# Kernel tuning notes

Hardware: AMD Instinct MI355X
Metric: run time of the kernel (lower is better)

The kernel has to match this reference:

```python
import jax, jax.numpy as jnp
import numpy as np

ITERATIONS = 20  # Resonator(iterations=20)
B, F, V, D = 128, 4, 2048, 4096


def _hardsign(x):
    # bipolar normalization used by MAP-VSA multiset(normalize=True); ties -> +1
    return jnp.where(x >= 0, 1.0, -1.0).astype(x.dtype)


def setup_inputs() -> dict:
    key = jax.random.key(0)
    k1, k2 = jax.random.split(key, 2)
    # bipolar codebooks: (F, V, D)
    codebooks = _hardsign(jax.random.normal(k1, (F, V, D), dtype=jnp.float32))
    # a realistic composite input: bind (elementwise product) of one codevector per factor
    idx = jax.random.randint(k2, (B, F), 0, V)                       # (B, F)
    chosen = codebooks[jnp.arange(F)[None, :], idx]                  # (B, F, D)
    inputs = jnp.prod(chosen, axis=1)                                # (B, D)
    # standard resonator init: normalized superposition of each codebook
    init_estimates = jnp.broadcast_to(
        _hardsign(jnp.sum(codebooks, axis=1)), (B, F, D)
    ).astype(jnp.float32)                                            # (B, F, D)
    return {"inputs": inputs, "init_estimates": init_estimates, "codebooks": codebooks}


def _resonator_step(inputs, est, codebooks):
    # est: (B, F, D). rolled stack over k=1..F-1 -> (B, F, F-1, D)
    f = est.shape[-2]
    rolled = jnp.stack([jnp.roll(est, k, axis=-2) for k in range(1, f)], axis=-2)
    inv_others = jnp.prod(rolled, axis=-2)          # multibind over dim -2 -> (B, F, D)
    new_est = inputs[:, None, :] * inv_others       # bind -> (B, F, D)
    sim = jnp.einsum('bfd,fvd->bfv', new_est, codebooks)   # similarity (activation='NONE')
    # multiset(codebooks, sim, normalize=True)
    return _hardsign(jnp.einsum('bfv,fvd->bfd', sim, codebooks))


def reference(inputs, init_estimates, codebooks):
    def body(carry, i):
        est, k, done = carry
        new = _resonator_step(inputs, est, codebooks)
        eq = jnp.all(new == est)          # convergence check (fixed point)
        k = jnp.where(done, k, i)
        return (new, k, done | eq), None

    carry0 = (init_estimates, jnp.int32(0), jnp.bool_(False))
    (est, k, _), _ = jax.lax.scan(body, carry0, jnp.arange(ITERATIONS, dtype=jnp.int32))
    # cleanup: argmax of |similarity| per factor (argmax_abs=True)
    sim = jnp.einsum('bfd,fvd->bfv', est, codebooks)
    outcome = jnp.argmax(jnp.abs(sim), axis=-1)     # (B, F) int indices
    return outcome, k
```

## Files before the change

### kernel.cpp

```cpp
#include <hip/hip_runtime.h>
#include <stdint.h>

#define B_    128
#define F_    4
#define V_    2048
#define D_    4096
#define DW    64
#define VW    32
#define ITERS 20
#define NKT   16
#define NBLK  512
#define ESLOT (B_ * F_ * DW)
#define SSLOT ((size_t)F_ * B_ * V_)

typedef _Float16 half8 __attribute__((ext_vector_type(8)));
typedef float   floatx4 __attribute__((ext_vector_type(4)));

__device__ __forceinline__ void cstore64(uint64_t* p, uint64_t v) {
    __hip_atomic_store(p, v, __ATOMIC_RELAXED, __HIP_MEMORY_SCOPE_AGENT);
}
__device__ __forceinline__ void cstore32(uint32_t* p, uint32_t v) {
    __hip_atomic_store(p, v, __ATOMIC_RELAXED, __HIP_MEMORY_SCOPE_AGENT);
}

__device__ __forceinline__ void xbar(int* bar, int gen) {
    __syncthreads();
    if (threadIdx.x == 0) {
        int s = blockIdx.x & 15;
        int t = __hip_atomic_fetch_add(&bar[s * 16], 1, __ATOMIC_RELAXED,
                                       __HIP_MEMORY_SCOPE_AGENT);
        if (t == gen * (NBLK / 16) - 1)
            __hip_atomic_fetch_add(&bar[256], 1, __ATOMIC_RELAXED,
                                   __HIP_MEMORY_SCOPE_AGENT);
        int spins = 0;
        if (blockIdx.x < 8) {
            while (__hip_atomic_load(&bar[256], __ATOMIC_RELAXED,
                                     __HIP_MEMORY_SCOPE_AGENT) < gen * 16) {
                __builtin_amdgcn_s_sleep(2);
                if (++spins > (1 << 16)) break;
            }
            __hip_atomic_store(&bar[288 + blockIdx.x * 32], gen,
                               __ATOMIC_RELAXED, __HIP_MEMORY_SCOPE_AGENT);
        } else {
            while (__hip_atomic_load(&bar[288 + (blockIdx.x & 7) * 32],
                                     __ATOMIC_RELAXED,
                                     __HIP_MEMORY_SCOPE_AGENT) < gen) {
                __builtin_amdgcn_s_sleep(2);
                if (++spins > (1 << 16)) break;
            }
        }
    }
    __syncthreads();
}

__device__ __forceinline__ void pack32c(const float* __restrict__ x,
                                        uint32_t* __restrict__ bits, int t) {
    const float4* p = (const float4*)x + (size_t)t * 8;
    uint32_t m = 0;
    #pragma unroll
    for (int j = 0; j < 8; ++j) {
        float4 v = p[j];
        m |= (__float_as_uint(v.x) >> 31) << (4 * j + 0);
        m |= (__float_as_uint(v.y) >> 31) << (4 * j + 1);
        m |= (__float_as_uint(v.z) >> 31) << (4 * j + 2);
        m |= (__float_as_uint(v.w) >> 31) << (4 * j + 3);
    }
    cstore32(&bits[t], m);
}

__global__ __launch_bounds__(256, 2) void k_loop(
        const float* __restrict__ cbf, const float* __restrict__ inite,
        const float* __restrict__ inputs,
        uint64_t* __restrict__ cb_bits, uint64_t* __restrict__ cbT,
        uint64_t* __restrict__ est_base, uint64_t* __restrict__ in_bits,
        _Float16* __restrict__ simf_base, int* __restrict__ flags,
        int* __restrict__ keys, int* __restrict__ out, int* bar) {
    const int bid = blockIdx.x;
    const int tid = threadIdx.x;
    const int gtid = bid * 256 + tid;
    int g = 0;

    __shared__ __align__(16) unsigned char LDSU[65536];
    __shared__ uint64_t LUT16[16];
    __shared__ int bd;

    if (tid < 16) {
        uint64_t e = 0;
        #pragma unroll
        for (int j = 0; j < 4; ++j)
            e |= (((tid >> j) & 1) ? 0xBC00ull : 0x3C00ull) << (16 * j);
        LUT16[tid] = e;
    }

    {
        const int ncb = (F_ * V_ * D_) / 32;
        for (int t = gtid; t < ncb; t += NBLK * 256)
            pack32c(cbf, (uint32_t*)cb_bits, t);
        if (gtid < (B_ * F_ * D_) / 32) pack32c(inite, (uint32_t*)est_base, gtid);
        if (gtid < (B_ * D_) / 32)      pack32c(inputs, (uint32_t*)in_bits, gtid);
        if (gtid < 32)      cstore32((uint32_t*)&flags[gtid], 0);
        if (gtid < B_ * F_) cstore32((uint32_t*)&keys[gtid], 0);
    }
    xbar(bar, ++g);

    {
        int wave = tid >> 6, lane = tid & 63;
        #pragma unroll 1
        for (int s = 0; s < 4; ++s) {
            int u = (bid * 4 + wave) + 2048 * s;
            int vw = u & 31, dw = (u >> 5) & 63, f = u >> 11;
            uint64_t w = cb_bits[((size_t)f * V_ + vw * 64 + lane) * DW + dw];
            uint64_t r = 0;
            for (int d2 = 0; d2 < 64; ++d2) {
                uint64_t m = __ballot((unsigned)((w >> d2) & 1));
                if (lane == d2) r = m;
            }
            cstore64(&cbT[((size_t)f * D_ + dw * 64 + lane) * VW + vw], r);
        }
    }
    xbar(bar, ++g);

    const int sgrp = bid & 7;
    const int s_bt = sgrp & 3, s_fhi = sgrp >> 2;
    const int shi  = bid >> 3;
    const int s_vt = shi & 31, s_flo = shi >> 5;
    const int s_f  = s_fhi + 2 * s_flo;
    const int s_v0 = s_vt * 64, s_b0 = s_bt * 32;

    const int ggrp = bid & 7;
    const int g_mt = ggrp & 1, g_f = ggrp >> 1;
    const int g_nt = bid >> 3;
    const int g_m0 = g_mt * 64, g_n0 = g_nt * 64;

    ulonglong2* CB2 = (ulonglong2*)LDSU;
    ulonglong2* NB2 = (ulonglong2*)(LDSU + 32768);
    _Float16*   As  = (_Float16*)(LDSU + 32768);
    uint64_t*   Bb  = (uint64_t*)(LDSU + 49152);

    #pragma unroll
    for (int it = 0; it < 8; ++it) {
        int cq = it * 256 + tid;
        int r = cq >> 5, ch = cq & 31;
        const ulonglong2* src = (const ulonglong2*)(cb_bits + ((size_t)s_f * V_ + s_v0 + r) * DW);
        CB2[r * 32 + (ch ^ (r & 7))] = src[ch];
    }
    {
        const uint64_t* bsrc = cbT + ((size_t)g_f * D_ + g_n0) * VW;
        #pragma unroll
        for (int p = 0; p < 4; ++p) {
            int chunk = p * 256 + tid;
            int dloc = chunk >> 4, cw = chunk & 15;
            ulonglong2 val = *(const ulonglong2*)&bsrc[dloc * VW + cw * 2];
            *(ulonglong2*)&Bb[dloc * VW + ((cw ^ (dloc & 15)) * 2)] = val;
        }
    }

    #pragma unroll 1
    for (int i = 0; i < ITERS; ++i) {
        const uint64_t* esti = est_base + (size_t)i * ESLOT;
        uint64_t*       esto = est_base + (size_t)(i + 1) * ESLOT;
        _Float16*       simf = simf_base + (size_t)i * SSLOT;

        {
            #pragma unroll
            for (int it = 0; it < 4; ++it) {
                int cq = it * 256 + tid;
                int r = cq >> 5, ch = cq & 31;
                int b = s_b0 + r;
                const ulonglong2* iv = (const ulonglong2*)(in_bits + (size_t)b * DW);
                const uint64_t* eb = esti + (size_t)b * F_ * DW;
                ulonglong2 i2 = iv[ch];
                ulonglong2 e0 = ((const ulonglong2*)(eb + 0 * DW))[ch];
                ulonglong2 e1 = ((const ulonglong2*)(eb + 1 * DW))[ch];
                ulonglong2 e2 = ((const ulonglong2*)(eb + 2 * DW))[ch];
                ulonglong2 e3 = ((const ulonglong2*)(eb + 3 * DW))[ch];
                uint64_t ex = (s_f == 0) ? e0.x : (s_f == 1) ? e1.x : (s_f == 2) ? e2.x : e3.x;
                uint64_t ey = (s_f == 0) ? e0.y : (s_f == 1) ? e1.y : (s_f == 2) ? e2.y : e3.y;
                ulonglong2 val;
                val.x = i2.x ^ e0.x ^ e1.x ^ e2.x ^ e3.x ^ ex;
                val.y = i2.y ^ e0.y ^ e1.y ^ e2.y ^ e3.y ^ ey;
                NB2[r * 32 + (ch ^ (r & 7))] = val;
            }
            __syncthreads();

            int vv = tid & 15, bb = tid >> 4;
            int svz = vv & 7, sbz = bb & 7;
            int pc[2][4];
            #pragma unroll
            for (int j = 0; j < 2; ++j)
                #pragma unroll
                for (int ii = 0; ii < 4; ++ii) pc[j][ii] = 0;

            #pragma unroll 4
            for (int ch = 0; ch < 32; ++ch) {
                ulonglong2 c[4], n[2];
                #pragma unroll
                for (int ii = 0; ii < 4; ++ii)
                    c[ii] = CB2[(vv + 16 * ii) * 32 + (ch ^ svz)];
                #pragma unroll
                for (int j = 0; j < 2; ++j)
                    n[j] = NB2[(bb + 16 * j) * 32 + (ch ^ sbz)];
                #pragma unroll
                for (int j = 0; j < 2; ++j)
                    #pragma unroll
                    for (int ii = 0; ii < 4; ++ii)
                        pc[j][ii] += __popcll(n[j].x ^ c[ii].x) + __popcll(n[j].y ^ c[ii].y);
            }
            #pragma unroll
            for (int j = 0; j < 2; ++j) {
                int b = s_b0 + bb + 16 * j;
                #pragma unroll
                for (int ii = 0; ii < 4; ++ii) {
                    int v = s_v0 + vv + 16 * ii;
                    union { _Float16 hf; unsigned short us; } cv;
                    cv.hf = (_Float16)(2048 - pc[j][ii]);
                    int other = __shfl_xor((int)cv.us, 1, 64);
                    if (!(vv & 1)) {
                        uint32_t packv = (uint32_t)cv.us | ((uint32_t)other << 16);
                        cstore32((uint32_t*)&simf[((size_t)s_f * B_ + b) * V_ + v], packv);
                    }
                }
            }
        }
        xbar(bar, ++g);

        {
            int lane = tid & 63, wave = tid >> 6;
            int lrow = lane & 15, lq = lane >> 4;
            int wm = wave & 1, wn = wave >> 1;
            if (tid == 0) bd = 0;

            const _Float16* Ab = simf + (size_t)g_f * B_ * V_ + (size_t)g_m0 * V_;
            int arow = tid >> 4, acol = tid & 15;
            half8 areg[4];
            #pragma unroll
            for (int p = 0; p < 4; ++p)
                areg[p] = *(const half8*)&Ab[(size_t)(p * 16 + arow) * V_ + acol * 8];

            floatx4 acc[2][2] = {};

            #pragma unroll 1
            for (int kt = 0; kt < NKT; ++kt) {
                __syncthreads();
                #pragma unroll
                for (int p = 0; p < 4; ++p)
                    *(half8*)&As[(p * 16 + arow) * 128 + ((acol ^ arow) * 8)] = areg[p];
                if (kt + 1 < NKT) {
                    #pragma unroll
                    for (int p = 0; p < 4; ++p)
                        areg[p] = *(const half8*)&Ab[(size_t)(p * 16 + arow) * V_ + (kt + 1) * 128 + acol * 8];
                }
                __syncthreads();

                ulonglong2 bw[2];
                #pragma unroll
                for (int nt2 = 0; nt2 < 2; ++nt2) {
                    int dloc = wn * 32 + nt2 * 16 + lrow;
                    bw[nt2] = *(const ulonglong2*)&Bb[dloc * VW + ((kt ^ (dloc & 15)) * 2)];
                }
                #pragma unroll
                for (int ks = 0; ks < 4; ++ks) {
                    half8 af[2];
                    #pragma unroll
                    for (int mt2 = 0; mt2 < 2; ++mt2) {
                        int row = wm * 32 + mt2 * 16 + lrow;
                        af[mt2] = *(const half8*)&As[row * 128 + (((ks * 4 + lq) ^ lrow) * 8)];
                    }
                    half8 bfrag[2];
                    #pragma unroll
                    for (int nt2 = 0; nt2 < 2; ++nt2) {
                        uint64_t w = (ks < 2) ? bw[nt2].x : bw[nt2].y;
                        uint32_t byte = (uint32_t)(w >> ((((ks & 1) * 4 + lq)) * 8)) & 0xFFu;
                        union { uint64_t q[2]; half8 h; } bu;
                        bu.q[0] = LUT16[byte & 0xFu];
                        bu.q[1] = LUT16[byte >> 4];
                        bfrag[nt2] = bu.h;
                    }
                    #pragma unroll
                    for (int mt2 = 0; mt2 < 2; ++mt2)
                        #pragma unroll
                        for (int nt2 = 0; nt2 < 2; ++nt2)
                            acc[mt2][nt2] = __builtin_amdgcn_mfma_f32_16x16x32_f16(
                                af[mt2], bfrag[nt2], acc[mt2][nt2], 0, 0, 0);
                }
            }

            __syncthreads();
            unsigned char* S = (unsigned char*)As;
            #pragma unroll
            for (int mt2 = 0; mt2 < 2; ++mt2)
                #pragma unroll
                for (int nt2 = 0; nt2 < 2; ++nt2)
                    #pragma unroll
                    for (int r = 0; r < 4; ++r) {
                        int row = wm * 32 + mt2 * 16 + lq * 4 + r;
                        int col = wn * 32 + nt2 * 16 + lrow;
                        S[row * 64 + col] = (acc[mt2][nt2][r] < 0.0f) ? 1 : 0;
                    }
            __syncthreads();
            if (tid < 64) {
                const uint64_t* Sw = (const uint64_t*)S;
                uint64_t m = 0;
                #pragma unroll
                for (int j = 0; j < 8; ++j) {
                    uint64_t w = Sw[tid * 8 + j];
                    m |= ((w * 0x0102040810204080ull) >> 56) << (8 * j);
                }
                size_t widx = ((size_t)(g_m0 + tid) * F_ + g_f) * DW + g_nt;
                uint64_t old = esti[widx];
                cstore64(&esto[widx], m);
                if (old != m) atomicOr(&bd, 1);
            }
            __syncthreads();
            if (tid == 0 && bd) atomicOr(&flags[i], 1);
        }
        xbar(bar, ++g);
    }

    {
        const uint64_t* estF = est_base + (size_t)ITERS * ESLOT;
        int vt = bid & 63, bg = (bid >> 6) & 1, f = bid >> 7;
        int v0 = vt * 32, b0g = bg * 64;
        ulonglong2* EB2 = (ulonglong2*)LDSU;
        ulonglong2* CBa = (ulonglong2*)(LDSU + 32768);
        #pragma unroll
        for (int it = 0; it < 8; ++it) {
            int cq = it * 256 + tid;
            int r = cq >> 5, ch = cq & 31;
            const ulonglong2* src = (const ulonglong2*)(estF + ((size_t)(b0g + r) * F_ + f) * DW);
            EB2[r * 32 + (ch ^ (r & 7))] = src[ch];
        }
        #pragma unroll
        for (int it = 0; it < 4; ++it) {
            int cq = it * 256 + tid;
            int r = cq >> 5, ch = cq & 31;
            const ulonglong2* src = (const ulonglong2*)(cb_bits + ((size_t)f * V_ + v0 + r) * DW);
            CBa[r * 32 + (ch ^ (r & 7))] = src[ch];
        }
        __syncthreads();

        int vv = tid & 15, bb = tid >> 4;
        int svz = vv & 7, sbz = bb & 7;
        int pc[4][2];
        #pragma unroll
        for (int j = 0; j < 4; ++j) { pc[j][0] = 0; pc[j][1] = 0; }

        #pragma unroll 4
        for (int ch = 0; ch < 32; ++ch) {
            ulonglong2 c[2], n[4];
            #pragma unroll
            for (int ii = 0; ii < 2; ++ii)
                c[ii] = CBa[(vv + 16 * ii) * 32 + (ch ^ svz)];
            #pragma unroll
            for (int j = 0; j < 4; ++j)
                n[j] = EB2[(bb + 16 * j) * 32 + (ch ^ sbz)];
            #pragma unroll
            for (int j = 0; j < 4; ++j)
                #pragma unroll
                for (int ii = 0; ii < 2; ++ii)
                    pc[j][ii] += __popcll(n[j].x ^ c[ii].x) + __popcll(n[j].y ^ c[ii].y);
        }
        #pragma unroll
        for (int j = 0; j < 4; ++j) {
            int kj = (int)0x80000000;
            #pragma unroll
            for (int ii = 0; ii < 2; ++ii) {
                int v = v0 + vv + 16 * ii;
                int m = 2048 - pc[j][ii]; if (m < 0) m = -m;
                int key = (m << 11) | (2047 - v);
                if (key > kj) kj = key;
            }
            #pragma unroll
            for (int s = 1; s < 16; s <<= 1) {
                int o = __shfl_xor(kj, s, 64);
                if (o > kj) kj = o;
            }
            if ((tid & 15) == 0)
                atomicMax(&keys[(size_t)(b0g + bb + 16 * j) * F_ + f], kj);
        }
    }
    xbar(bar, ++g);

    if (bid == 0) {
        for (int t = tid; t < B_ * F_; t += 256)
            cstore32((uint32_t*)&out[t], (uint32_t)(2047 - (keys[t] & 0x7FF)));
        if (tid == 0) {
            int k = ITERS - 1;
            for (int i2 = 0; i2 < ITERS; ++i2)
                if (flags[i2] == 0) { k = i2; break; }
            cstore32((uint32_t*)&out[B_ * F_], (uint32_t)k);
        }
    }
}

extern "C" void kernel_launch(void* const* d_in, const int* in_sizes, int n_in,
                              void* d_out, int out_size, void* d_ws, size_t ws_size,
                              hipStream_t stream) {
    const float* inputs = (const float*)d_in[0];
    const float* inite  = (const float*)d_in[1];
    const float* cb     = (const float*)d_in[2];
    int* out = (int*)d_out;

    char* ws = (char*)d_ws;
    uint64_t* cb_bits  = (uint64_t*)ws;  ws += (size_t)F_ * V_ * DW * 8;
    uint64_t* cbT_bits = (uint64_t*)ws;  ws += (size_t)F_ * D_ * VW * 8;
    uint64_t* est_base = (uint64_t*)ws;  ws += (size_t)(ITERS + 1) * ESLOT * 8;
    uint64_t* in_bits  = (uint64_t*)ws;  ws += (size_t)B_ * DW * 8;
    _Float16* simf     = (_Float16*)ws;  ws += (size_t)ITERS * SSLOT * 2;
    int*      flags    = (int*)ws;       ws += 32 * 4;
    int*      keys     = (int*)ws;       ws += B_ * F_ * 4;
    int*      bar      = (int*)ws;       ws += 4096;

    hipMemsetAsync(bar, 0, 4096, stream);

    k_loop<<<NBLK, 256, 0, stream>>>(cb, inite, inputs, cb_bits, cbT_bits,
                                     est_base, in_bits, simf, flags, keys,
                                     out, bar);
}
```

Before: 845.1 us.

## Halve persistent grid to 256 blocks with doubled per-block tiles and ALU fp16 expansion

Cuts the persistent cooperative grid from 512 to 256 blocks and doubles each block's work in every phase: the popcount similarity tile covers 64 batch rows, the MFMA tile covers 128 d-columns, and the final argmax covers all batch rows. This halves the participants in every grid barrier, and there are about two dozen barriers per launch, while raising operand reuse per block. In exchange, occupancy drops to one 256-thread block per CU and LDS grows to 96 KB. The shared-memory LUT for bit-to-fp16 expansion is replaced by a multiply/mask/xor sequence.

```diff
diff --git a/kernel.cpp b/kernel.cpp
--- a/kernel.cpp
+++ b/kernel.cpp
@@ -9,7 +9,7 @@
 #define VW    32
 #define ITERS 20
 #define NKT   16
-#define NBLK  512
+#define NBLK  256
 #define ESLOT (B_ * F_ * DW)
 #define SSLOT ((size_t)F_ * B_ * V_)
 
@@ -68,7 +68,7 @@
     cstore32(&bits[t], m);
 }
 
-__global__ __launch_bounds__(256, 2) void k_loop(
+__global__ __launch_bounds__(256) void k_loop(
         const float* __restrict__ cbf, const float* __restrict__ inite,
         const float* __restrict__ inputs,
         uint64_t* __restrict__ cb_bits, uint64_t* __restrict__ cbT,
@@ -80,17 +80,8 @@
     const int gtid = bid * 256 + tid;
     int g = 0;
 
-    __shared__ __align__(16) unsigned char LDSU[65536];
-    __shared__ uint64_t LUT16[16];
+    __shared__ __align__(16) unsigned char LDSU[98304];
     __shared__ int bd;
-
-    if (tid < 16) {
-        uint64_t e = 0;
-        #pragma unroll
-        for (int j = 0; j < 4; ++j)
-            e |= (((tid >> j) & 1) ? 0xBC00ull : 0x3C00ull) << (16 * j);
-        LUT16[tid] = e;
-    }
 
     {
         const int ncb = (F_ * V_ * D_) / 32;
@@ -106,8 +97,8 @@
     {
         int wave = tid >> 6, lane = tid & 63;
         #pragma unroll 1
-        for (int s = 0; s < 4; ++s) {
-            int u = (bid * 4 + wave) + 2048 * s;
+        for (int s = 0; s < 8; ++s) {
+            int u = (bid * 4 + wave) + 1024 * s;
             int vw = u & 31, dw = (u >> 5) & 63, f = u >> 11;
             uint64_t w = cb_bits[((size_t)f * V_ + vw * 64 + lane) * DW + dw];
             uint64_t r = 0;
@@ -121,21 +112,19 @@
     xbar(bar, ++g);
 
     const int sgrp = bid & 7;
-    const int s_bt = sgrp & 3, s_fhi = sgrp >> 2;
-    const int shi  = bid >> 3;
-    const int s_vt = shi & 31, s_flo = shi >> 5;
-    const int s_f  = s_fhi + 2 * s_flo;
-    const int s_v0 = s_vt * 64, s_b0 = s_bt * 32;
+    const int s_bt = sgrp & 1, s_f = sgrp >> 1;
+    const int s_vt = bid >> 3;
+    const int s_v0 = s_vt * 64, s_b0 = s_bt * 64;
 
     const int ggrp = bid & 7;
     const int g_mt = ggrp & 1, g_f = ggrp >> 1;
     const int g_nt = bid >> 3;
-    const int g_m0 = g_mt * 64, g_n0 = g_nt * 64;
+    const int g_m0 = g_mt * 64, g_n0 = g_nt * 128;
 
     ulonglong2* CB2 = (ulonglong2*)LDSU;
-    ulonglong2* NB2 = (ulonglong2*)(LDSU + 32768);
-    _Float16*   As  = (_Float16*)(LDSU + 32768);
-    uint64_t*   Bb  = (uint64_t*)(LDSU + 49152);
+    uint64_t*   Bb  = (uint64_t*)(LDSU + 32768);
+    ulonglong2* NB2 = (ulonglong2*)(LDSU + 65536);
+    _Float16*   As  = (_Float16*)(LDSU + 65536);
 
     #pragma unroll
     for (int it = 0; it < 8; ++it) {
@@ -147,13 +136,17 @@
     {
         const uint64_t* bsrc = cbT + ((size_t)g_f * D_ + g_n0) * VW;
         #pragma unroll
-        for (int p = 0; p < 4; ++p) {
+        for (int p = 0; p < 8; ++p) {
             int chunk = p * 256 + tid;
             int dloc = chunk >> 4, cw = chunk & 15;
             ulonglong2 val = *(const ulonglong2*)&bsrc[dloc * VW + cw * 2];
             *(ulonglong2*)&Bb[dloc * VW + ((cw ^ (dloc & 15)) * 2)] = val;
         }
     }
+
+    const uint64_t SPREAD = 0x1000200040008000ull;
+    const uint64_t SMASK  = 0x8000800080008000ull;
+    const uint64_t PONE   = 0x3C003C003C003C00ull;
 
     #pragma unroll 1
     for (int i = 0; i < ITERS; ++i) {
@@ -163,7 +156,7 @@
 
         {
             #pragma unroll
-            for (int it = 0; it < 4; ++it) {
+            for (int it = 0; it < 8; ++it) {
                 int cq = it * 256 + tid;
                 int r = cq >> 5, ch = cq & 31;
                 int b = s_b0 + r;
@@ -185,29 +178,29 @@
 
             int vv = tid & 15, bb = tid >> 4;
             int svz = vv & 7, sbz = bb & 7;
-            int pc[2][4];
-            #pragma unroll
-            for (int j = 0; j < 2; ++j)
+            int pc[4][4];
+            #pragma unroll
+            for (int j = 0; j < 4; ++j)
                 #pragma unroll
                 for (int ii = 0; ii < 4; ++ii) pc[j][ii] = 0;
 
             #pragma unroll 4
             for (int ch = 0; ch < 32; ++ch) {
-                ulonglong2 c[4], n[2];
+                ulonglong2 c[4], n[4];
                 #pragma unroll
                 for (int ii = 0; ii < 4; ++ii)
                     c[ii] = CB2[(vv + 16 * ii) * 32 + (ch ^ svz)];
                 #pragma unroll
-                for (int j = 0; j < 2; ++j)
+                for (int j = 0; j < 4; ++j)
                     n[j] = NB2[(bb + 16 * j) * 32 + (ch ^ sbz)];
                 #pragma unroll
-                for (int j = 0; j < 2; ++j)
+                for (int j = 0; j < 4; ++j)
                     #pragma unroll
                     for (int ii = 0; ii < 4; ++ii)
                         pc[j][ii] += __popcll(n[j].x ^ c[ii].x) + __popcll(n[j].y ^ c[ii].y);
             }
             #pragma unroll
-            for (int j = 0; j < 2; ++j) {
+            for (int j = 0; j < 4; ++j) {
                 int b = s_b0 + bb + 16 * j;
                 #pragma unroll
                 for (int ii = 0; ii < 4; ++ii) {
@@ -237,7 +230,7 @@
             for (int p = 0; p < 4; ++p)
                 areg[p] = *(const half8*)&Ab[(size_t)(p * 16 + arow) * V_ + acol * 8];
 
-            floatx4 acc[2][2] = {};
+            floatx4 acc[2][4] = {};
 
             #pragma unroll 1
             for (int kt = 0; kt < NKT; ++kt) {
@@ -252,10 +245,10 @@
                 }
                 __syncthreads();
 
-                ulonglong2 bw[2];
-                #pragma unroll
-                for (int nt2 = 0; nt2 < 2; ++nt2) {
-                    int dloc = wn * 32 + nt2 * 16 + lrow;
+                ulonglong2 bw[4];
+                #pragma unroll
+                for (int nt2 = 0; nt2 < 4; ++nt2) {
+                    int dloc = wn * 64 + nt2 * 16 + lrow;
                     bw[nt2] = *(const ulonglong2*)&Bb[dloc * VW + ((kt ^ (dloc & 15)) * 2)];
                 }
                 #pragma unroll
@@ -266,20 +259,20 @@
                         int row = wm * 32 + mt2 * 16 + lrow;
                         af[mt2] = *(const half8*)&As[row * 128 + (((ks * 4 + lq) ^ lrow) * 8)];
                     }
-                    half8 bfrag[2];
-                    #pragma unroll
-                    for (int nt2 = 0; nt2 < 2; ++nt2) {
+                    half8 bfrag[4];
+                    #pragma unroll
+                    for (int nt2 = 0; nt2 < 4; ++nt2) {
                         uint64_t w = (ks < 2) ? bw[nt2].x : bw[nt2].y;
                         uint32_t byte = (uint32_t)(w >> ((((ks & 1) * 4 + lq)) * 8)) & 0xFFu;
                         union { uint64_t q[2]; half8 h; } bu;
-                        bu.q[0] = LUT16[byte & 0xFu];
-                        bu.q[1] = LUT16[byte >> 4];
+                        bu.q[0] = (((uint64_t)(byte & 0xFu) * SPREAD) & SMASK) ^ PONE;
+                        bu.q[1] = (((uint64_t)(byte >> 4)   * SPREAD) & SMASK) ^ PONE;
                         bfrag[nt2] = bu.h;
                     }
                     #pragma unroll
                     for (int mt2 = 0; mt2 < 2; ++mt2)
                         #pragma unroll
-                        for (int nt2 = 0; nt2 < 2; ++nt2)
+                        for (int nt2 = 0; nt2 < 4; ++nt2)
                             acc[mt2][nt2] = __builtin_amdgcn_mfma_f32_16x16x32_f16(
                                 af[mt2], bfrag[nt2], acc[mt2][nt2], 0, 0, 0);
                 }
@@ -290,23 +283,24 @@
             #pragma unroll
             for (int mt2 = 0; mt2 < 2; ++mt2)
                 #pragma unroll
-                for (int nt2 = 0; nt2 < 2; ++nt2)
+                for (int nt2 = 0; nt2 < 4; ++nt2)
                     #pragma unroll
                     for (int r = 0; r < 4; ++r) {
                         int row = wm * 32 + mt2 * 16 + lq * 4 + r;
-                        int col = wn * 32 + nt2 * 16 + lrow;
-                        S[row * 64 + col] = (acc[mt2][nt2][r] < 0.0f) ? 1 : 0;
+                        int col = wn * 64 + nt2 * 16 + lrow;
+                        S[row * 128 + col] = (acc[mt2][nt2][r] < 0.0f) ? 1 : 0;
                     }
             __syncthreads();
-            if (tid < 64) {
+            if (tid < 128) {
+                int row = tid >> 1, half = tid & 1;
                 const uint64_t* Sw = (const uint64_t*)S;
                 uint64_t m = 0;
                 #pragma unroll
                 for (int j = 0; j < 8; ++j) {
-                    uint64_t w = Sw[tid * 8 + j];
+                    uint64_t w = Sw[row * 16 + half * 8 + j];
                     m |= ((w * 0x0102040810204080ull) >> 56) << (8 * j);
                 }
-                size_t widx = ((size_t)(g_m0 + tid) * F_ + g_f) * DW + g_nt;
+                size_t widx = ((size_t)(g_m0 + row) * F_ + g_f) * DW + g_nt * 2 + half;
                 uint64_t old = esti[widx];
                 cstore64(&esto[widx], m);
                 if (old != m) atomicOr(&bd, 1);
@@ -319,15 +313,15 @@
 
     {
         const uint64_t* estF = est_base + (size_t)ITERS * ESLOT;
-        int vt = bid & 63, bg = (bid >> 6) & 1, f = bid >> 7;
-        int v0 = vt * 32, b0g = bg * 64;
+        int vt = bid & 63, f = bid >> 6;
+        int v0 = vt * 32;
         ulonglong2* EB2 = (ulonglong2*)LDSU;
-        ulonglong2* CBa = (ulonglong2*)(LDSU + 32768);
+        ulonglong2* CBa = (ulonglong2*)(LDSU + 65536);
         #pragma unroll
-        for (int it = 0; it < 8; ++it) {
+        for (int it = 0; it < 16; ++it) {
             int cq = it * 256 + tid;
             int r = cq >> 5, ch = cq & 31;
-            const ulonglong2* src = (const ulonglong2*)(estF + ((size_t)(b0g + r) * F_ + f) * DW);
+            const ulonglong2* src = (const ulonglong2*)(estF + ((size_t)r * F_ + f) * DW);
             EB2[r * 32 + (ch ^ (r & 7))] = src[ch];
         }
         #pragma unroll
@@ -341,27 +335,27 @@
 
         int vv = tid & 15, bb = tid >> 4;
         int svz = vv & 7, sbz = bb & 7;
-        int pc[4][2];
+        int pc[8][2];
         #pragma unroll
-        for (int j = 0; j < 4; ++j) { pc[j][0] = 0; pc[j][1] = 0; }
+        for (int j = 0; j < 8; ++j) { pc[j][0] = 0; pc[j][1] = 0; }
 
         #pragma unroll 4
         for (int ch = 0; ch < 32; ++ch) {
-            ulonglong2 c[2], n[4];
+            ulonglong2 c[2], n[8];
             #pragma unroll
             for (int ii = 0; ii < 2; ++ii)
                 c[ii] = CBa[(vv + 16 * ii) * 32 + (ch ^ svz)];
             #pragma unroll
-            for (int j = 0; j < 4; ++j)
+            for (int j = 0; j < 8; ++j)
                 n[j] = EB2[(bb + 16 * j) * 32 + (ch ^ sbz)];
             #pragma unroll
-            for (int j = 0; j < 4; ++j)
+            for (int j = 0; j < 8; ++j)
                 #pragma unroll
                 for (int ii = 0; ii < 2; ++ii)
                     pc[j][ii] += __popcll(n[j].x ^ c[ii].x) + __popcll(n[j].y ^ c[ii].y);
         }
         #pragma unroll
-        for (int j = 0; j < 4; ++j) {
+        for (int j = 0; j < 8; ++j) {
             int kj = (int)0x80000000;
             #pragma unroll
             for (int ii = 0; ii < 2; ++ii) {
@@ -376,7 +370,7 @@
                 if (o > kj) kj = o;
             }
             if ((tid & 15) == 0)
-                atomicMax(&keys[(size_t)(b0g + bb + 16 * j) * F_ + f], kj);
+                atomicMax(&keys[(size_t)(bb + 16 * j) * F_ + f], kj);
         }
     }
     xbar(bar, ++g);
```

New measurement: 933.8 us. 10.5% more time.

## Align sim and GEMM block partitions and replace grid barriers with group barriers

Applied to the files above, without the earlier changes.

Remaps the similarity stage so each block computes sim for the same (batch-half, factor) tile it later consumes in the projection GEMM, with a 64-row by 32-v tile instead of 32 by 64. This lets the full-grid barrier after the sim stage become a barrier over just the 64 blocks sharing that (mt, f) group. The barrier after the GEMM becomes a barrier over the 256 blocks sharing the batch half. The goal is to cut global synchronisation latency per iteration. In exchange, each block loads twice as many batch rows of estimates per iteration, and the barriers use a single shared atomic counter that is more contended.

```diff
diff --git a/kernel.cpp b/kernel.cpp
--- a/kernel.cpp
+++ b/kernel.cpp
@@ -53,6 +53,24 @@
     __syncthreads();
 }
 
+__device__ __forceinline__ void gbar(int* cnt, int* flag, int members, int gen) {
+    __syncthreads();
+    if (threadIdx.x == 0) {
+        int t = __hip_atomic_fetch_add(cnt, 1, __ATOMIC_RELAXED,
+                                       __HIP_MEMORY_SCOPE_AGENT);
+        if (t == gen * members - 1)
+            __hip_atomic_store(flag, gen, __ATOMIC_RELAXED,
+                               __HIP_MEMORY_SCOPE_AGENT);
+        int spins = 0;
+        while (__hip_atomic_load(flag, __ATOMIC_RELAXED,
+                                 __HIP_MEMORY_SCOPE_AGENT) < gen) {
+            __builtin_amdgcn_s_sleep(2);
+            if (++spins > (1 << 16)) break;
+        }
+    }
+    __syncthreads();
+}
+
 __device__ __forceinline__ void pack32c(const float* __restrict__ x,
                                         uint32_t* __restrict__ bits, int t) {
     const float4* p = (const float4*)x + (size_t)t * 8;
@@ -78,7 +96,7 @@
     const int bid = blockIdx.x;
     const int tid = threadIdx.x;
     const int gtid = bid * 256 + tid;
-    int g = 0;
+    int g = 0, gs = 0, gh = 0;
 
     __shared__ __align__(16) unsigned char LDSU[65536];
     __shared__ uint64_t LUT16[16];
@@ -120,32 +138,32 @@
     }
     xbar(bar, ++g);
 
-    const int sgrp = bid & 7;
-    const int s_bt = sgrp & 3, s_fhi = sgrp >> 2;
-    const int shi  = bid >> 3;
-    const int s_vt = shi & 31, s_flo = shi >> 5;
-    const int s_f  = s_fhi + 2 * s_flo;
-    const int s_v0 = s_vt * 64, s_b0 = s_bt * 32;
-
-    const int ggrp = bid & 7;
-    const int g_mt = ggrp & 1, g_f = ggrp >> 1;
-    const int g_nt = bid >> 3;
-    const int g_m0 = g_mt * 64, g_n0 = g_nt * 64;
+    const int x  = bid & 7;
+    const int mt = x & 1, f = x >> 1;
+    const int nt = bid >> 3;
+    const int m0 = mt * 64;
+    const int n0 = nt * 64;
+    const int v0 = nt * 32;
+
+    int* scnt = &bar[576 + x * 32];
+    int* sflg = &bar[576 + x * 32 + 16];
+    int* hcnt = &bar[832 + mt * 32];
+    int* hflg = &bar[832 + mt * 32 + 16];
 
     ulonglong2* CB2 = (ulonglong2*)LDSU;
+    uint64_t*   Bb  = (uint64_t*)(LDSU + 16384);
     ulonglong2* NB2 = (ulonglong2*)(LDSU + 32768);
     _Float16*   As  = (_Float16*)(LDSU + 32768);
-    uint64_t*   Bb  = (uint64_t*)(LDSU + 49152);
 
     #pragma unroll
-    for (int it = 0; it < 8; ++it) {
+    for (int it = 0; it < 4; ++it) {
         int cq = it * 256 + tid;
         int r = cq >> 5, ch = cq & 31;
-        const ulonglong2* src = (const ulonglong2*)(cb_bits + ((size_t)s_f * V_ + s_v0 + r) * DW);
+        const ulonglong2* src = (const ulonglong2*)(cb_bits + ((size_t)f * V_ + v0 + r) * DW);
         CB2[r * 32 + (ch ^ (r & 7))] = src[ch];
     }
     {
-        const uint64_t* bsrc = cbT + ((size_t)g_f * D_ + g_n0) * VW;
+        const uint64_t* bsrc = cbT + ((size_t)f * D_ + n0) * VW;
         #pragma unroll
         for (int p = 0; p < 4; ++p) {
             int chunk = p * 256 + tid;
@@ -163,10 +181,10 @@
 
         {
             #pragma unroll
-            for (int it = 0; it < 4; ++it) {
+            for (int it = 0; it < 8; ++it) {
                 int cq = it * 256 + tid;
                 int r = cq >> 5, ch = cq & 31;
-                int b = s_b0 + r;
+                int b = m0 + r;
                 const ulonglong2* iv = (const ulonglong2*)(in_bits + (size_t)b * DW);
                 const uint64_t* eb = esti + (size_t)b * F_ * DW;
                 ulonglong2 i2 = iv[ch];
@@ -174,8 +192,8 @@
                 ulonglong2 e1 = ((const ulonglong2*)(eb + 1 * DW))[ch];
                 ulonglong2 e2 = ((const ulonglong2*)(eb + 2 * DW))[ch];
                 ulonglong2 e3 = ((const ulonglong2*)(eb + 3 * DW))[ch];
-                uint64_t ex = (s_f == 0) ? e0.x : (s_f == 1) ? e1.x : (s_f == 2) ? e2.x : e3.x;
-                uint64_t ey = (s_f == 0) ? e0.y : (s_f == 1) ? e1.y : (s_f == 2) ? e2.y : e3.y;
+                uint64_t ex = (f == 0) ? e0.x : (f == 1) ? e1.x : (f == 2) ? e2.x : e3.x;
+                uint64_t ey = (f == 0) ? e0.y : (f == 1) ? e1.y : (f == 2) ? e2.y : e3.y;
                 ulonglong2 val;
                 val.x = i2.x ^ e0.x ^ e1.x ^ e2.x ^ e3.x ^ ex;
                 val.y = i2.y ^ e0.y ^ e1.y ^ e2.y ^ e3.y ^ ey;
@@ -185,44 +203,44 @@
 
             int vv = tid & 15, bb = tid >> 4;
             int svz = vv & 7, sbz = bb & 7;
-            int pc[2][4];
-            #pragma unroll
-            for (int j = 0; j < 2; ++j)
-                #pragma unroll
-                for (int ii = 0; ii < 4; ++ii) pc[j][ii] = 0;
+            int pc[4][2];
+            #pragma unroll
+            for (int j = 0; j < 4; ++j)
+                #pragma unroll
+                for (int ii = 0; ii < 2; ++ii) pc[j][ii] = 0;
 
             #pragma unroll 4
             for (int ch = 0; ch < 32; ++ch) {
-                ulonglong2 c[4], n[2];
-                #pragma unroll
-                for (int ii = 0; ii < 4; ++ii)
+                ulonglong2 c[2], n[4];
+                #pragma unroll
+                for (int ii = 0; ii < 2; ++ii)
                     c[ii] = CB2[(vv + 16 * ii) * 32 + (ch ^ svz)];
                 #pragma unroll
-                for (int j = 0; j < 2; ++j)
+                for (int j = 0; j < 4; ++j)
                     n[j] = NB2[(bb + 16 * j) * 32 + (ch ^ sbz)];
                 #pragma unroll
-                for (int j = 0; j < 2; ++j)
-                    #pragma unroll
-                    for (int ii = 0; ii < 4; ++ii)
+                for (int j = 0; j < 4; ++j)
+                    #pragma unroll
+                    for (int ii = 0; ii < 2; ++ii)
                         pc[j][ii] += __popcll(n[j].x ^ c[ii].x) + __popcll(n[j].y ^ c[ii].y);
             }
             #pragma unroll
-            for (int j = 0; j < 2; ++j) {
-                int b = s_b0 + bb + 16 * j;
-                #pragma unroll
-                for (int ii = 0; ii < 4; ++ii) {
-                    int v = s_v0 + vv + 16 * ii;
+            for (int j = 0; j < 4; ++j) {
+                int b = m0 + bb + 16 * j;
+                #pragma unroll
+                for (int ii = 0; ii < 2; ++ii) {
+                    int v = v0 + vv + 16 * ii;
                     union { _Float16 hf; unsigned short us; } cv;
                     cv.hf = (_Float16)(2048 - pc[j][ii]);
                     int other = __shfl_xor((int)cv.us, 1, 64);
                     if (!(vv & 1)) {
                         uint32_t packv = (uint32_t)cv.us | ((uint32_t)other << 16);
-                        cstore32((uint32_t*)&simf[((size_t)s_f * B_ + b) * V_ + v], packv);
+                        cstore32((uint32_t*)&simf[((size_t)f * B_ + b) * V_ + v], packv);
                     }
                 }
             }
         }
-        xbar(bar, ++g);
+        gbar(scnt, sflg, 64, ++gs);
 
         {
             int lane = tid & 63, wave = tid >> 6;
@@ -230,7 +248,7 @@
             int wm = wave & 1, wn = wave >> 1;
             if (tid == 0) bd = 0;
 
-            const _Float16* Ab = simf + (size_t)g_f * B_ * V_ + (size_t)g_m0 * V_;
+            const _Float16* Ab = simf + (size_t)f * B_ * V_ + (size_t)m0 * V_;
             int arow = tid >> 4, acol = tid & 15;
             half8 areg[4];
             #pragma unroll
@@ -306,7 +324,7 @@
                     uint64_t w = Sw[tid * 8 + j];
                     m |= ((w * 0x0102040810204080ull) >> 56) << (8 * j);
                 }
-                size_t widx = ((size_t)(g_m0 + tid) * F_ + g_f) * DW + g_nt;
+                size_t widx = ((size_t)(m0 + tid) * F_ + f) * DW + nt;
                 uint64_t old = esti[widx];
                 cstore64(&esto[widx], m);
                 if (old != m) atomicOr(&bd, 1);
@@ -314,27 +332,29 @@
             __syncthreads();
             if (tid == 0 && bd) atomicOr(&flags[i], 1);
         }
-        xbar(bar, ++g);
-    }
+        gbar(hcnt, hflg, 256, ++gh);
+    }
+
+    xbar(bar, ++g);
 
     {
         const uint64_t* estF = est_base + (size_t)ITERS * ESLOT;
-        int vt = bid & 63, bg = (bid >> 6) & 1, f = bid >> 7;
-        int v0 = vt * 32, b0g = bg * 64;
+        int vt = bid & 63, bg = (bid >> 6) & 1, fa = bid >> 7;
+        int av0 = vt * 32, b0g = bg * 64;
         ulonglong2* EB2 = (ulonglong2*)LDSU;
         ulonglong2* CBa = (ulonglong2*)(LDSU + 32768);
         #pragma unroll
         for (int it = 0; it < 8; ++it) {
             int cq = it * 256 + tid;
             int r = cq >> 5, ch = cq & 31;
-            const ulonglong2* src = (const ulonglong2*)(estF + ((size_t)(b0g + r) * F_ + f) * DW);
+            const ulonglong2* src = (const ulonglong2*)(estF + ((size_t)(b0g + r) * F_ + fa) * DW);
             EB2[r * 32 + (ch ^ (r & 7))] = src[ch];
         }
         #pragma unroll
         for (int it = 0; it < 4; ++it) {
             int cq = it * 256 + tid;
             int r = cq >> 5, ch = cq & 31;
-            const ulonglong2* src = (const ulonglong2*)(cb_bits + ((size_t)f * V_ + v0 + r) * DW);
+            const ulonglong2* src = (const ulonglong2*)(cb_bits + ((size_t)fa * V_ + av0 + r) * DW);
             CBa[r * 32 + (ch ^ (r & 7))] = src[ch];
         }
         __syncthreads();
@@ -365,7 +385,7 @@
             int kj = (int)0x80000000;
             #pragma unroll
             for (int ii = 0; ii < 2; ++ii) {
-                int v = v0 + vv + 16 * ii;
+                int v = av0 + vv + 16 * ii;
                 int m = 2048 - pc[j][ii]; if (m < 0) m = -m;
                 int key = (m << 11) | (2047 - v);
                 if (key > kj) kj = key;
@@ -376,7 +396,7 @@
                 if (o > kj) kj = o;
             }
             if ((tid & 15) == 0)
-                atomicMax(&keys[(size_t)(b0g + bb + 16 * j) * F_ + f], kj);
+                atomicMax(&keys[(size_t)(b0g + bb + 16 * j) * F_ + fa], kj);
         }
     }
     xbar(bar, ++g);
```

New measurement: 937.9 us. 11.0% more time.
